# Performance work log

Hardware: AMD Instinct MI355X
Metric: run time of the kernel (lower is better)

The kernel has to match this reference:

```python
import jax, jax.numpy as jnp
import numpy as np

N_NODES = 50000
N_EDGES = 1600000
IN_DIM = 256
OUT_DIM = 128
T = 8
V_THRESHOLD = 1.0
TAU = 2.0
STEP_SIZE = 0.1


def setup_inputs() -> dict:
    key = jax.random.key(0)
    k1, k2, k3 = jax.random.split(key, 3)
    x = jax.random.normal(k1, (N_NODES, IN_DIM), dtype=jnp.float32)
    W = jax.random.normal(k2, (IN_DIM, OUT_DIM), dtype=jnp.float32) / np.sqrt(IN_DIM)
    edge_index = jax.random.randint(k3, (2, N_EDGES), 0, N_NODES, dtype=jnp.int64)
    return {"x": x, "W": W, "edge_index": edge_index}


def gcn_conv(x, W, edge_index):
    # GCNConv (no bias): h = D^{-1/2} (A + I) D^{-1/2} (x @ W)
    n = x.shape[0]
    h = x @ W  # [N, OUT]
    loops = jnp.arange(n, dtype=edge_index.dtype)
    src = jnp.concatenate([edge_index[0], loops])
    dst = jnp.concatenate([edge_index[1], loops])
    deg = jax.ops.segment_sum(jnp.ones_like(dst, dtype=h.dtype), dst, num_segments=n)
    dinv = jnp.where(deg > 0, jax.lax.rsqrt(deg), 0.0)
    norm = dinv[src] * dinv[dst]  # [E+N]
    msgs = h[src] * norm[:, None]
    return jax.ops.segment_sum(msgs, dst, num_segments=n)  # [N, OUT]


def reference(x, W, edge_index):
    h = gcn_conv(x, W, edge_index)            # encoder output, [N, OUT]
    u = h * STEP_SIZE                          # per-step tangent input
    z0 = jnp.zeros_like(h)                     # manifold origin

    def step(z, _):
        # leaky charge toward input current, fire on threshold, soft reset
        Hm = z + (u - z) / TAU
        o = (Hm >= V_THRESHOLD).astype(Hm.dtype)
        z_new = Hm - o * V_THRESHOLD
        return z_new, (o, z_new)

    _, (o_seq, z_seq) = jax.lax.scan(step, z0, None, length=T)
    return o_seq, z_seq  # each [T, N, OUT]
```

## Files before the change

### kernel.cpp

```cpp
#include <hip/hip_runtime.h>
#include <hip/hip_bf16.h>

#define N_NODES 50000
#define N_EDGES 1600000
#define IN_DIM  256
#define OUT_DIM 128
#define T_STEPS 8

typedef __attribute__((ext_vector_type(8))) short bf16x8;
typedef __attribute__((ext_vector_type(4))) float f32x4;


__device__ inline unsigned short bf_hi_trunc(float x) {
    return (unsigned short)(__float_as_uint(x) >> 16);
}
__device__ inline float bf_to_f(unsigned short u) {
    return __uint_as_float((unsigned)u << 16);
}
__device__ inline unsigned short f2bf_rne(float a) {
    __hip_bfloat16 t = __float2bfloat16(a);
    return *(unsigned short*)&t;
}
__device__ inline float bf_lo(unsigned p) { return __uint_as_float(p << 16); }
__device__ inline float bf_hi(unsigned p) { return __uint_as_float(p & 0xffff0000u); }

__global__ __launch_bounds__(256) void
k_prep_count(const float* __restrict__ W,
             unsigned short* __restrict__ Wt_hi,
             unsigned short* __restrict__ Wt_lo,
             const int* __restrict__ edge, int* __restrict__ cnt) {
    int idx = blockIdx.x * 256 + threadIdx.x;
    const int4* dst4 = (const int4*)(edge + N_EDGES);
    for (int e = idx; e < N_EDGES / 4; e += 800 * 256) {
        int4 d = dst4[e];
        atomicAdd(&cnt[d.x], 1);
        atomicAdd(&cnt[d.y], 1);
        atomicAdd(&cnt[d.z], 1);
        atomicAdd(&cnt[d.w], 1);
    }
    if (idx < 32768) {
        int n = idx >> 8;
        int k = idx & 255;
        float w = W[k * OUT_DIM + n];
        unsigned short hi = bf_hi_trunc(w);
        Wt_hi[idx] = hi;
        Wt_lo[idx] = f2bf_rne(w - bf_to_f(hi));
    }
}

__global__ __launch_bounds__(256) void
k_scanA(const int* __restrict__ cnt, int* __restrict__ part) {
    int t = threadIdx.x;
    int i4 = blockIdx.x * 256 + t;
    int4 v = make_int4(0, 0, 0, 0);
    if (i4 < 12500) v = ((const int4*)cnt)[i4];
    int s = v.x + v.y + v.z + v.w;
    __shared__ int sd[256];
    sd[t] = s; __syncthreads();
    for (int o = 128; o > 0; o >>= 1) {
        if (t < o) sd[t] += sd[t + o];
        __syncthreads();
    }
    if (t == 0) part[blockIdx.x] = sd[0];
}

__global__ void k_scanB(int* __restrict__ part) {
    int l = threadIdx.x;
    int v = (l < 49) ? part[l] : 0;
    int orig = v;
    for (int o = 1; o < 64; o <<= 1) {
        int u = __shfl_up(v, o);
        if (l >= o) v += u;
    }
    if (l < 49) part[l] = v - orig;
}

__global__ __launch_bounds__(256) void
k_scanC(const int* __restrict__ cnt, const int* __restrict__ part,
        int* __restrict__ offs, int* __restrict__ fill,
        float* __restrict__ dinv) {
    int t = threadIdx.x;
    int i4 = blockIdx.x * 256 + t;
    int4 v = make_int4(0, 0, 0, 0);
    if (i4 < 12500) v = ((const int4*)cnt)[i4];
    int s = v.x + v.y + v.z + v.w;
    __shared__ int sd[256];
    sd[t] = s; __syncthreads();
    for (int o = 1; o < 256; o <<= 1) {
        int u = (t >= o) ? sd[t - o] : 0;
        __syncthreads();
        sd[t] += u;
        __syncthreads();
    }
    if (i4 < 12500) {
        int base = part[blockIdx.x] + sd[t] - s;
        int4 o4;
        o4.x = base;
        o4.y = o4.x + v.x;
        o4.z = o4.y + v.y;
        o4.w = o4.z + v.z;
        ((int4*)offs)[i4] = o4;
        ((int4*)fill)[i4] = o4;
        float4 d4;
        d4.x = rsqrtf((float)(v.x + 1));
        d4.y = rsqrtf((float)(v.y + 1));
        d4.z = rsqrtf((float)(v.z + 1));
        d4.w = rsqrtf((float)(v.w + 1));
        ((float4*)dinv)[i4] = d4;
    }
}

__global__ __launch_bounds__(256) void
k_gemm(const float* __restrict__ x,
       const unsigned short* __restrict__ Wt_hi,
       const unsigned short* __restrict__ Wt_lo,
       const float* __restrict__ dinv,
       unsigned short* __restrict__ hs) {
    int wave = blockIdx.x * 4 + (threadIdx.x >> 6);
    if (wave >= N_NODES / 16) return;
    int lane = threadIdx.x & 63;
    int quad = lane >> 4;
    int r16  = lane & 15;
    int m0 = wave * 16;

    f32x4 acc[8];
#pragma unroll
    for (int nt = 0; nt < 8; ++nt) acc[nt] = (f32x4){0.f, 0.f, 0.f, 0.f};

#pragma unroll
    for (int kt = 0; kt < 8; ++kt) {
        int k0 = kt * 32 + quad * 8;
        const float* xp = x + (size_t)(m0 + r16) * IN_DIM + k0;
        float4 v0 = *(const float4*)xp;
        float4 v1 = *(const float4*)(xp + 4);
        float vv[8] = {v0.x, v0.y, v0.z, v0.w, v1.x, v1.y, v1.z, v1.w};
        union { bf16x8 v; unsigned short u[8]; } ahi, alo;
#pragma unroll
        for (int j = 0; j < 8; ++j) {
            unsigned short hi = bf_hi_trunc(vv[j]);
            ahi.u[j] = hi;
            alo.u[j] = f2bf_rne(vv[j] - bf_to_f(hi));
        }
#pragma unroll
        for (int nt = 0; nt < 8; ++nt) {
            size_t woff = (size_t)(nt * 16 + r16) * IN_DIM + k0;
            bf16x8 bhi = *(const bf16x8*)(Wt_hi + woff);
            bf16x8 blo = *(const bf16x8*)(Wt_lo + woff);
            acc[nt] = __builtin_amdgcn_mfma_f32_16x16x32_bf16(ahi.v, bhi, acc[nt], 0, 0, 0);
            acc[nt] = __builtin_amdgcn_mfma_f32_16x16x32_bf16(alo.v, bhi, acc[nt], 0, 0, 0);
            acc[nt] = __builtin_amdgcn_mfma_f32_16x16x32_bf16(ahi.v, blo, acc[nt], 0, 0, 0);
        }
    }
    float dr[4];
#pragma unroll
    for (int r = 0; r < 4; ++r) dr[r] = dinv[m0 + quad * 4 + r];
#pragma unroll
    for (int nt = 0; nt < 8; ++nt) {
#pragma unroll
        for (int r = 0; r < 4; ++r) {
            int row = m0 + quad * 4 + r;
            int col = nt * 16 + r16;
            hs[(size_t)row * OUT_DIM + col] = f2bf_rne(acc[nt][r] * dr[r]);
        }
    }
}

__global__ __launch_bounds__(256) void
k_fill(const int* __restrict__ edge, int* __restrict__ fill,
       int* __restrict__ csr) {
    int e4 = blockIdx.x * 256 + threadIdx.x;
    if (e4 < N_EDGES / 4) {
        int4 s = ((const int4*)edge)[e4];
        int4 d = ((const int4*)(edge + N_EDGES))[e4];
        int p;
        p = atomicAdd(&fill[d.x], 1); csr[p] = s.x;
        p = atomicAdd(&fill[d.y], 1); csr[p] = s.y;
        p = atomicAdd(&fill[d.z], 1); csr[p] = s.z;
        p = atomicAdd(&fill[d.w], 1); csr[p] = s.w;
    }
}

__global__ __launch_bounds__(256) void
k_agg_snn(const unsigned* __restrict__ hs,
          const int* __restrict__ offs, const int* __restrict__ cnt,
          const float* __restrict__ dinv, const int* __restrict__ csr,
          float* __restrict__ out) {
    int node = blockIdx.x * 4 + (threadIdx.x >> 6);
    int lane = threadIdx.x & 63;

    unsigned p = hs[node * 64 + lane];
    float a0 = bf_lo(p), a1 = bf_hi(p);

    int beg = __builtin_amdgcn_readfirstlane(offs[node]);
    int end = __builtin_amdgcn_readfirstlane(offs[node] + cnt[node]);
    int j = beg;
    for (; j + 8 <= end; j += 8) {
        int s0 = csr[j+0], s1 = csr[j+1], s2 = csr[j+2], s3 = csr[j+3];
        int s4 = csr[j+4], s5 = csr[j+5], s6 = csr[j+6], s7 = csr[j+7];
        unsigned q0 = hs[s0*64+lane], q1 = hs[s1*64+lane];
        unsigned q2 = hs[s2*64+lane], q3 = hs[s3*64+lane];
        unsigned q4 = hs[s4*64+lane], q5 = hs[s5*64+lane];
        unsigned q6 = hs[s6*64+lane], q7 = hs[s7*64+lane];
        a0 += bf_lo(q0); a1 += bf_hi(q0);
        a0 += bf_lo(q1); a1 += bf_hi(q1);
        a0 += bf_lo(q2); a1 += bf_hi(q2);
        a0 += bf_lo(q3); a1 += bf_hi(q3);
        a0 += bf_lo(q4); a1 += bf_hi(q4);
        a0 += bf_lo(q5); a1 += bf_hi(q5);
        a0 += bf_lo(q6); a1 += bf_hi(q6);
        a0 += bf_lo(q7); a1 += bf_hi(q7);
    }
    for (; j < end; ++j) {
        int s = csr[j];
        unsigned q = hs[s*64+lane];
        a0 += bf_lo(q); a1 += bf_hi(q);
    }

    float di = dinv[node];
    float u0 = a0 * di * 0.1f, u1 = a1 * di * 0.1f;
    float z0 = 0.f, z1 = 0.f;
    float2* out2 = (float2*)out;
    size_t baseo = (size_t)node * 64 + lane;
    const size_t plane = (size_t)N_NODES * 64;
    union F2U { float2 f; unsigned long long u; };
#pragma unroll
    for (int t = 0; t < T_STEPS; ++t) {
        float H0 = z0 + (u0 - z0) * 0.5f;
        float H1 = z1 + (u1 - z1) * 0.5f;
        float o0 = (H0 >= 1.0f) ? 1.0f : 0.0f;
        float o1 = (H1 >= 1.0f) ? 1.0f : 0.0f;
        z0 = H0 - o0;
        z1 = H1 - o1;
        F2U a, b;
        a.f = make_float2(o0, o1);
        b.f = make_float2(z0, z1);
        __builtin_nontemporal_store(a.u,
            (unsigned long long*)(out2 + (size_t)t * plane + baseo));
        __builtin_nontemporal_store(b.u,
            (unsigned long long*)(out2 + (size_t)(T_STEPS + t) * plane + baseo));
    }
}

extern "C" void kernel_launch(void* const* d_in, const int* in_sizes, int n_in,
                              void* d_out, int out_size, void* d_ws, size_t ws_size,
                              hipStream_t stream) {
    const float* x  = (const float*)d_in[0];
    const float* W  = (const float*)d_in[1];
    const int*   ei = (const int*)d_in[2];
    float* out = (float*)d_out;

    char* ws = (char*)d_ws;
    unsigned short* hs    = (unsigned short*)(ws + 0);
    unsigned short* Wt_hi = (unsigned short*)(ws + 12800000);
    unsigned short* Wt_lo = (unsigned short*)(ws + 12865536);
    int*            cnt   = (int*)(ws + 12931072);
    int*            fill  = (int*)(ws + 13131072);
    int*            offs  = (int*)(ws + 13331072);
    float*          dinv  = (float*)(ws + 13531072);
    int*            part  = (int*)(ws + 13731072);
    int*            csr   = (int*)(ws + 13731328);

    hipMemsetAsync(cnt, 0, 200000, stream);

    k_prep_count<<<800, 256, 0, stream>>>(W, Wt_hi, Wt_lo, ei, cnt);
    k_scanA<<<49, 256, 0, stream>>>(cnt, part);
    k_scanB<<<1, 64, 0, stream>>>(part);
    k_scanC<<<49, 256, 0, stream>>>(cnt, part, offs, fill, dinv);
    k_gemm<<<782, 256, 0, stream>>>(x, Wt_hi, Wt_lo, dinv, hs);
    k_fill<<<1563, 256, 0, stream>>>(ei, fill, csr);
    k_agg_snn<<<12500, 256, 0, stream>>>((const unsigned*)hs, offs, cnt, dinv, csr, out);
}
```

Baseline: 705.2 us.

## Split edge gather across half-waves with 16-bit CSR and vector output stores

The CSR source indices are stored as 16-bit values, which fit because the node count is below 65536. This halves CSR write and read traffic. In the aggregation kernel each half-wave now handles alternate edges with 8-byte loads per lane, so two neighbor rows are in flight per step, and the halves are combined with a cross-lane shuffle. The output phase writes one 16-byte nontemporal store per lane per step, with the lower half writing spikes and the upper half writing membrane states. The cost is extra odd/even edge handling and shuffle work, plus a hard dependence on node indices fitting in 16 bits.

Result: no change. 708.9 us (+0.5%).

```diff
diff --git a/kernel.cpp b/kernel.cpp
--- a/kernel.cpp
+++ b/kernel.cpp
@@ -167,77 +167,113 @@
 
 __global__ __launch_bounds__(256) void
 k_fill(const int* __restrict__ edge, int* __restrict__ fill,
-       int* __restrict__ csr) {
+       unsigned short* __restrict__ csr) {
     int e4 = blockIdx.x * 256 + threadIdx.x;
     if (e4 < N_EDGES / 4) {
         int4 s = ((const int4*)edge)[e4];
         int4 d = ((const int4*)(edge + N_EDGES))[e4];
         int p;
-        p = atomicAdd(&fill[d.x], 1); csr[p] = s.x;
-        p = atomicAdd(&fill[d.y], 1); csr[p] = s.y;
-        p = atomicAdd(&fill[d.z], 1); csr[p] = s.z;
-        p = atomicAdd(&fill[d.w], 1); csr[p] = s.w;
-    }
-}
-
-__global__ __launch_bounds__(256) void
-k_agg_snn(const unsigned* __restrict__ hs,
+        p = atomicAdd(&fill[d.x], 1); csr[p] = (unsigned short)s.x;
+        p = atomicAdd(&fill[d.y], 1); csr[p] = (unsigned short)s.y;
+        p = atomicAdd(&fill[d.z], 1); csr[p] = (unsigned short)s.z;
+        p = atomicAdd(&fill[d.w], 1); csr[p] = (unsigned short)s.w;
+    }
+}
+
+__global__ __launch_bounds__(256) void
+k_agg_snn(const unsigned short* __restrict__ hs,
           const int* __restrict__ offs, const int* __restrict__ cnt,
-          const float* __restrict__ dinv, const int* __restrict__ csr,
+          const float* __restrict__ dinv,
+          const unsigned short* __restrict__ csr,
           float* __restrict__ out) {
     int node = blockIdx.x * 4 + (threadIdx.x >> 6);
     int lane = threadIdx.x & 63;
-
-    unsigned p = hs[node * 64 + lane];
-    float a0 = bf_lo(p), a1 = bf_hi(p);
+    bool hi  = (lane >= 32);
+    int  loff = (lane & 31) * 8;
+    const char* hsb = (const char*)hs;
+
+    uint2 qs = *(const uint2*)(hsb + (size_t)node * 256 + loff);
+    float a0 = hi ? bf_lo(qs.x) : 0.f;
+    float a1 = hi ? bf_hi(qs.x) : 0.f;
+    float a2 = hi ? bf_lo(qs.y) : 0.f;
+    float a3 = hi ? bf_hi(qs.y) : 0.f;
 
     int beg = __builtin_amdgcn_readfirstlane(offs[node]);
     int end = __builtin_amdgcn_readfirstlane(offs[node] + cnt[node]);
+
     int j = beg;
-    for (; j + 8 <= end; j += 8) {
-        int s0 = csr[j+0], s1 = csr[j+1], s2 = csr[j+2], s3 = csr[j+3];
-        int s4 = csr[j+4], s5 = csr[j+5], s6 = csr[j+6], s7 = csr[j+7];
-        unsigned q0 = hs[s0*64+lane], q1 = hs[s1*64+lane];
-        unsigned q2 = hs[s2*64+lane], q3 = hs[s3*64+lane];
-        unsigned q4 = hs[s4*64+lane], q5 = hs[s5*64+lane];
-        unsigned q6 = hs[s6*64+lane], q7 = hs[s7*64+lane];
-        a0 += bf_lo(q0); a1 += bf_hi(q0);
-        a0 += bf_lo(q1); a1 += bf_hi(q1);
-        a0 += bf_lo(q2); a1 += bf_hi(q2);
-        a0 += bf_lo(q3); a1 += bf_hi(q3);
-        a0 += bf_lo(q4); a1 += bf_hi(q4);
-        a0 += bf_lo(q5); a1 += bf_hi(q5);
-        a0 += bf_lo(q6); a1 += bf_hi(q6);
-        a0 += bf_lo(q7); a1 += bf_hi(q7);
-    }
-    for (; j < end; ++j) {
-        int s = csr[j];
-        unsigned q = hs[s*64+lane];
-        a0 += bf_lo(q); a1 += bf_hi(q);
-    }
+    if (j & 1) {
+        unsigned s = csr[j];
+        if (!hi) {
+            uint2 q = *(const uint2*)(hsb + (size_t)s * 256 + loff);
+            a0 += bf_lo(q.x); a1 += bf_hi(q.x);
+            a2 += bf_lo(q.y); a3 += bf_hi(q.y);
+        }
+        ++j;
+    }
+    int nd = (end - j) >> 1;
+    const unsigned* cw = (const unsigned*)(csr + j);
+    int k = 0;
+    for (; k + 8 <= nd; k += 8) {
+        unsigned d[8];
+#pragma unroll
+        for (int q = 0; q < 8; ++q) d[q] = cw[k + q];
+        uint2 g[8];
+#pragma unroll
+        for (int q = 0; q < 8; ++q) {
+            unsigned s = hi ? (d[q] >> 16) : (d[q] & 0xffffu);
+            g[q] = *(const uint2*)(hsb + (size_t)s * 256 + loff);
+        }
+#pragma unroll
+        for (int q = 0; q < 8; ++q) {
+            a0 += bf_lo(g[q].x); a1 += bf_hi(g[q].x);
+            a2 += bf_lo(g[q].y); a3 += bf_hi(g[q].y);
+        }
+    }
+    for (; k < nd; ++k) {
+        unsigned d = cw[k];
+        unsigned s = hi ? (d >> 16) : (d & 0xffffu);
+        uint2 q = *(const uint2*)(hsb + (size_t)s * 256 + loff);
+        a0 += bf_lo(q.x); a1 += bf_hi(q.x);
+        a2 += bf_lo(q.y); a3 += bf_hi(q.y);
+    }
+    int jt = j + 2 * nd;
+    if (jt < end) {
+        unsigned s = csr[jt];
+        if (!hi) {
+            uint2 q = *(const uint2*)(hsb + (size_t)s * 256 + loff);
+            a0 += bf_lo(q.x); a1 += bf_hi(q.x);
+            a2 += bf_lo(q.y); a3 += bf_hi(q.y);
+        }
+    }
+
+    a0 += __shfl(a0, lane ^ 32);
+    a1 += __shfl(a1, lane ^ 32);
+    a2 += __shfl(a2, lane ^ 32);
+    a3 += __shfl(a3, lane ^ 32);
 
     float di = dinv[node];
     float u0 = a0 * di * 0.1f, u1 = a1 * di * 0.1f;
-    float z0 = 0.f, z1 = 0.f;
-    float2* out2 = (float2*)out;
-    size_t baseo = (size_t)node * 64 + lane;
-    const size_t plane = (size_t)N_NODES * 64;
-    union F2U { float2 f; unsigned long long u; };
+    float u2 = a2 * di * 0.1f, u3 = a3 * di * 0.1f;
+    float z0 = 0.f, z1 = 0.f, z2 = 0.f, z3 = 0.f;
+
+    const size_t plane = (size_t)N_NODES * 128;
+    size_t base = (size_t)node * 128 + (size_t)(lane & 31) * 4
+                + (hi ? (size_t)T_STEPS * plane : 0);
 #pragma unroll
     for (int t = 0; t < T_STEPS; ++t) {
         float H0 = z0 + (u0 - z0) * 0.5f;
         float H1 = z1 + (u1 - z1) * 0.5f;
+        float H2 = z2 + (u2 - z2) * 0.5f;
+        float H3 = z3 + (u3 - z3) * 0.5f;
         float o0 = (H0 >= 1.0f) ? 1.0f : 0.0f;
         float o1 = (H1 >= 1.0f) ? 1.0f : 0.0f;
-        z0 = H0 - o0;
-        z1 = H1 - o1;
-        F2U a, b;
-        a.f = make_float2(o0, o1);
-        b.f = make_float2(z0, z1);
-        __builtin_nontemporal_store(a.u,
-            (unsigned long long*)(out2 + (size_t)t * plane + baseo));
-        __builtin_nontemporal_store(b.u,
-            (unsigned long long*)(out2 + (size_t)(T_STEPS + t) * plane + baseo));
+        float o2 = (H2 >= 1.0f) ? 1.0f : 0.0f;
+        float o3 = (H3 >= 1.0f) ? 1.0f : 0.0f;
+        z0 = H0 - o0; z1 = H1 - o1; z2 = H2 - o2; z3 = H3 - o3;
+        f32x4 v = {hi ? z0 : o0, hi ? z1 : o1,
+                   hi ? z2 : o2, hi ? z3 : o3};
+        __builtin_nontemporal_store(v, (f32x4*)(out + base + (size_t)t * plane));
     }
 }
 
@@ -258,7 +294,7 @@
     int*            offs  = (int*)(ws + 13331072);
     float*          dinv  = (float*)(ws + 13531072);
     int*            part  = (int*)(ws + 13731072);
-    int*            csr   = (int*)(ws + 13731328);
+    unsigned short* csr   = (unsigned short*)(ws + 13731328);
 
     hipMemsetAsync(cnt, 0, 200000, stream);
 
@@ -268,5 +304,5 @@
     k_scanC<<<49, 256, 0, stream>>>(cnt, part, offs, fill, dinv);
     k_gemm<<<782, 256, 0, stream>>>(x, Wt_hi, Wt_lo, dinv, hs);
     k_fill<<<1563, 256, 0, stream>>>(ei, fill, csr);
-    k_agg_snn<<<12500, 256, 0, stream>>>((const unsigned*)hs, offs, cnt, dinv, csr, out);
-}
+    k_agg_snn<<<12500, 256, 0, stream>>>(hs, offs, cnt, dinv, csr, out);
+}
```
